# Performance work log

Measured on AMD Instinct MI355X. Metric: run time of the kernel, lower is better.

## Reference

```python
import jax, jax.numpy as jnp
import numpy as np


def setup_inputs() -> dict:
    key = jax.random.key(0)
    k1, k2, k3 = jax.random.split(key, 3)
    B, T, D = 2, 2048, 1024
    x = jax.random.normal(k1, (B, T, D), dtype=jnp.float32)
    w_qkv = jax.random.normal(k2, (3 * D, D), dtype=jnp.float32) * (D ** -0.5)
    w_out = jax.random.normal(k3, (D, D), dtype=jnp.float32) * (D ** -0.5)
    return {"x": x, "w_qkv": w_qkv, "w_out": w_out, "heads": 16}


def reference(x, w_qkv, w_out, heads):
    # SelfAttention forward: attention_type='sdp', position_mode='alibi', causal=True, eval mode.
    B, T, D = x.shape
    H = heads
    hd = D // H
    scale = hd ** -0.5

    # qkv projection: torch Linear -> x @ W^T
    qkv = (x @ w_qkv.T).reshape(B, T, 3, H, hd)
    qkv = jnp.transpose(qkv, (2, 0, 3, 1, 4))  # [3, B, H, T, hd]
    q, k, v = qkv[0], qkv[1], qkv[2]

    # ALiBi relative bias: slopes = 1 / 2^(h/H) for h = 1..H
    slopes = 1.0 / jnp.power(2.0, jnp.arange(1, H + 1, dtype=jnp.float32) / H)
    pos = jnp.arange(T, dtype=jnp.float32)
    rel = jnp.abs(pos[:, None] - pos[None, :])  # [T, T]
    bias = -slopes[None, :, None, None] * rel[None, None, :, :]  # [1, H, T, T]

    # scores + causal mask + softmax (manual path since position_bias is not None)
    scores = jnp.einsum('bhqd,bhkd->bhqk', q, k) * scale + bias
    causal_mask = jnp.triu(jnp.ones((T, T), dtype=bool), k=1)
    scores = jnp.where(causal_mask[None, None, :, :], -jnp.inf, scores)
    attn = jax.nn.softmax(scores, axis=-1)
    attn = jnp.where(jnp.isnan(attn), 1.0 / float(max(T, 1)), attn)

    out = jnp.einsum('bhqk,bhkd->bhqd', attn, v)  # [B, H, T, hd]
    out = jnp.transpose(out, (0, 2, 1, 3)).reshape(B, T, D)
    return out @ w_out.T
```

## Files before the change

### kernel.cpp

```cpp
#include <hip/hip_runtime.h>
#include <hip/hip_bf16.h>

typedef __attribute__((ext_vector_type(8))) short shortx8;
typedef __attribute__((ext_vector_type(4))) float floatx4;
typedef __attribute__((ext_vector_type(4))) unsigned uintx4;
typedef __attribute__((ext_vector_type(2))) unsigned uintx2;

#define B_ 2
#define T_ 2048
#define D_ 1024
#define H_ 16
#define HD_ 64
#define SCALE 0.125f
#define QSCALE 0.18033688011112042f
#define SMAX2 23.083120654223414f
#define FULLH ((size_t)B_ * H_ * T_ * HD_)

#define GLDS16(g, l) __builtin_amdgcn_global_load_lds( \
    (__attribute__((address_space(1))) void*)(g), \
    (__attribute__((address_space(3))) void*)(l), 16, 0, 0)

__device__ __forceinline__ short f2bf(float f) {
    union { float f; unsigned u; } v; v.f = f;
    unsigned r = v.u + 0x7FFFu + ((v.u >> 16) & 1u);
    return (short)(r >> 16);
}

__device__ __forceinline__ unsigned pk2(float x, float y) {
    union { __hip_bfloat162 h; unsigned u; } t;
    t.h = __float22bfloat162_rn(make_float2(x, y));
    return t.u;
}

__device__ __forceinline__ shortx8 cvt8(floatx4 a, floatx4 b) {
    uintx4 r = { pk2(a[0], a[1]), pk2(a[2], a[3]), pk2(b[0], b[1]), pk2(b[2], b[3]) };
    return __builtin_bit_cast(shortx8, r);
}

__device__ __forceinline__ float ex2(float x) {
#if __has_builtin(__builtin_amdgcn_exp2f)
    return __builtin_amdgcn_exp2f(x);
#else
    return exp2f(x);
#endif
}

__global__ __launch_bounds__(256) void cvt_xw(const float* __restrict__ x,
                                              const float* __restrict__ wqkv,
                                              short* __restrict__ xbf,
                                              short* __restrict__ wbf) {
    int i = blockIdx.x * 256 + threadIdx.x;
    const float* src; short* dst; int o;
    if (i < 524288) { src = x; dst = xbf; o = i; }
    else            { src = wqkv; dst = wbf; o = i - 524288; }
    const floatx4* p = reinterpret_cast<const floatx4*>(src) + (size_t)o * 2;
    *(reinterpret_cast<shortx8*>(dst) + o) = cvt8(p[0], p[1]);
}


__global__ __launch_bounds__(256) void qkv_fast(const short* __restrict__ xbf,
                                                const short* __restrict__ wbf,
                                                short* __restrict__ qout,
                                                short* __restrict__ kv) {
    __shared__ __align__(16) short As[128 * 64];
    __shared__ __align__(16) short Bs[128 * 64];

    const int tid = threadIdx.x;
    const int wv = tid >> 6;
    const int l  = tid & 63;
    const int ln = l & 15;
    const int quad = l >> 4;
    const int rowb = quad << 2;
    const int wm = wv >> 1, wn = wv & 1;
    const int m0 = blockIdx.y * 128;
    const int n0g = blockIdx.x * 128;

    const int lr = l >> 3, lc = l & 7;
    const int gcol = (lc ^ lr) << 3;
    const short* agp = xbf + (size_t)(m0 + wv * 32 + lr) * D_ + gcol;
    const short* bgp = wbf + (size_t)(n0g + wv * 32 + lr) * D_ + gcol;
    short* aldsb = As + wv * 32 * 64;
    short* bldsb = Bs + wv * 32 * 64;

    floatx4 acc[4][4] = {};

    for (int k0 = 0; k0 < D_; k0 += 64) {
        __syncthreads();
#pragma unroll
        for (int c = 0; c < 4; ++c) {
            GLDS16(agp + (size_t)(c * 8) * D_ + k0, aldsb + c * 512);
            GLDS16(bgp + (size_t)(c * 8) * D_ + k0, bldsb + c * 512);
        }
        __syncthreads();

#pragma unroll
        for (int kk = 0; kk < 2; ++kk) {
            const int csw = (kk << 2) + quad;
            const int sw = (csw ^ (ln & 7)) << 3;
            shortx8 af[4], bf[4];
#pragma unroll
            for (int i = 0; i < 4; ++i)
                af[i] = *reinterpret_cast<const shortx8*>(&As[((wm * 64 + i * 16 + ln) << 6) + sw]);
#pragma unroll
            for (int j = 0; j < 4; ++j)
                bf[j] = *reinterpret_cast<const shortx8*>(&Bs[((wn * 64 + j * 16 + ln) << 6) + sw]);
#pragma unroll
            for (int i = 0; i < 4; ++i)
#pragma unroll
                for (int j = 0; j < 4; ++j)
                    acc[i][j] = __builtin_amdgcn_mfma_f32_16x16x32_bf16(af[i], bf[j], acc[i][j], 0, 0, 0);
        }
    }

    const int sel = n0g >> 10;
    const int bb = m0 >> 11;
    const int t0w = (m0 + wm * 64) & (T_ - 1);
    const int h = ((n0g + wn * 64) >> 6) & 15;

    if (sel < 2) {
        short* dst = (sel == 0) ? qout : kv;
        const float sc = (sel == 0) ? QSCALE : 1.0f;
        const size_t hb = (size_t)(bb * H_ + h) * T_;
#pragma unroll
        for (int i = 0; i < 4; ++i)
#pragma unroll
            for (int r = 0; r < 4; ++r) {
                int t = t0w + i * 16 + rowb + r;
#pragma unroll
                for (int j = 0; j < 4; ++j)
                    dst[(hb + t) * HD_ + j * 16 + ln] = f2bf(acc[i][j][r] * sc);
            }
    } else {
        __syncthreads();
        short* tb = (wv < 2) ? (As + wv * 4096) : (Bs + (wv - 2) * 4096);
        short* vhead = kv + FULLH + (size_t)(bb * H_ + h) * HD_ * T_;
        const int dl = l & 31, th = (l >> 5) << 5;
#pragma unroll
        for (int p = 0; p < 2; ++p) {
#pragma unroll
            for (int i = 0; i < 4; ++i)
#pragma unroll
                for (int jj = 0; jj < 2; ++jj) {
                    int j = 2 * p + jj;
#pragma unroll
                    for (int r = 0; r < 4; ++r)
                        tb[(jj * 16 + ln) * 72 + i * 16 + rowb + r] = f2bf(acc[i][j][r]);
                }
            short* vd = vhead + (size_t)(p * 32 + dl) * T_ + t0w + th;
#pragma unroll
            for (int seg = 0; seg < 4; ++seg)
                *reinterpret_cast<shortx8*>(vd + seg * 8) =
                    *reinterpret_cast<const shortx8*>(&tb[dl * 72 + th + seg * 8]);
        }
    }
}

__global__ __launch_bounds__(256) void out_fast(const short* __restrict__ Abf,
                                                const short* __restrict__ wbf,
                                                float* __restrict__ out) {
    __shared__ __align__(16) short As[128 * 64];
    __shared__ __align__(16) short Bs[128 * 64];

    const int tid = threadIdx.x;
    const int wv = tid >> 6;
    const int l  = tid & 63;
    const int ln = l & 15;
    const int quad = l >> 4;
    const int rowb = quad << 2;
    const int wm = wv >> 1, wn = wv & 1;
    const int m0 = blockIdx.y * 128;
    const int n0g = blockIdx.x * 128;

    const int lr = l >> 3, lc = l & 7;
    const int gcol = (lc ^ lr) << 3;
    const short* bgp = wbf + (size_t)(n0g + wv * 32 + lr) * D_ + gcol;
    short* aldsb = As + wv * 32 * 64;
    short* bldsb = Bs + wv * 32 * 64;

    size_t abase[4];
#pragma unroll
    for (int c = 0; c < 4; ++c) {
        int m = m0 + wv * 32 + c * 8 + lr;
        int bb2 = m >> 11, t = m & (T_ - 1);
        abase[c] = ((size_t)(bb2 * H_) * T_ + t) * HD_ + gcol;
    }

    floatx4 acc[4][4] = {};

    for (int k0 = 0; k0 < D_; k0 += 64) {
        const size_t hoff = (size_t)(k0 >> 6) * T_ * HD_;
        __syncthreads();
#pragma unroll
        for (int c = 0; c < 4; ++c) {
            GLDS16(Abf + abase[c] + hoff, aldsb + c * 512);
            GLDS16(bgp + (size_t)(c * 8) * D_ + k0, bldsb + c * 512);
        }
        __syncthreads();

#pragma unroll
        for (int kk = 0; kk < 2; ++kk) {
            const int csw = (kk << 2) + quad;
            const int sw = (csw ^ (ln & 7)) << 3;
            shortx8 af[4], bf[4];
#pragma unroll
            for (int i = 0; i < 4; ++i)
                af[i] = *reinterpret_cast<const shortx8*>(&As[((wm * 64 + i * 16 + ln) << 6) + sw]);
#pragma unroll
            for (int j = 0; j < 4; ++j)
                bf[j] = *reinterpret_cast<const shortx8*>(&Bs[((wn * 64 + j * 16 + ln) << 6) + sw]);
#pragma unroll
            for (int i = 0; i < 4; ++i)
#pragma unroll
                for (int j = 0; j < 4; ++j)
                    acc[i][j] = __builtin_amdgcn_mfma_f32_16x16x32_bf16(af[i], bf[j], acc[i][j], 0, 0, 0);
        }
    }

#pragma unroll
    for (int i = 0; i < 4; ++i)
#pragma unroll
        for (int r = 0; r < 4; ++r) {
            int m = m0 + wm * 64 + i * 16 + rowb + r;
#pragma unroll
            for (int j = 0; j < 4; ++j)
                out[(size_t)m * D_ + n0g + wn * 64 + j * 16 + ln] = acc[i][j][r];
        }
}

__global__ __launch_bounds__(256, 4) void attn(const short* __restrict__ qws,
                                               const short* __restrict__ kv,
                                               short* ao,
                                               const float* __restrict__ wout,
                                               short* __restrict__ wobf) {
    if (blockIdx.x >= 1024) {
        int i = (blockIdx.x - 1024) * 256 + threadIdx.x;
        const floatx4* p = reinterpret_cast<const floatx4*>(wout) + (size_t)i * 2;
        *(reinterpret_cast<shortx8*>(wobf) + i) = cvt8(p[0], p[1]);
        return;
    }

    __shared__ __align__(16) short Ks[64][72];
    __shared__ __align__(16) short Vt[64][72];
    __shared__ __align__(16) short Pt[4][64][18];

    const int tid = threadIdx.x;
    const int wv   = tid >> 6;
    const int l    = tid & 63;
    const int ln   = l & 15;
    const int quad = l >> 4;
    const int qd   = quad << 3;
    const int rowb = quad << 2;

    const int xcd  = blockIdx.x & 7;
    const int slot = blockIdx.x >> 3;
    const int bh   = xcd * 4 + (slot & 3);
    const int qb   = 31 - (slot >> 2);
    const int h    = bh & 15;
    const int b    = bh >> 4;

    const float slope2 = 1.4426950408889634f * exp2f(-(float)(h + 1) * 0.0625f);
    const size_t koff = (size_t)(b * H_ + h) * T_ * HD_;
    const int q0 = qb * 64 + wv * 16;

    shortx8 qf[2];
#pragma unroll
    for (int kk = 0; kk < 2; ++kk)
        qf[kk] = *reinterpret_cast<const shortx8*>(&qws[koff + (size_t)(q0 + ln) * HD_ + kk * 32 + qd]);

    const int r0 = tid >> 3, c0 = (tid & 7) << 3, r1 = r0 + 32;
    const short* kbase = kv + koff;
    const short* vbase = kv + FULLH + koff;
    shortx8 kA, kB, vA, vB;
    auto FETCH = [&](int kb) {
        const short* kp = kbase + ((size_t)(kb * 64) << 6);
        kA = *reinterpret_cast<const shortx8*>(kp + ((size_t)r0 << 6) + c0);
        kB = *reinterpret_cast<const shortx8*>(kp + ((size_t)r1 << 6) + c0);
        const short* vp = vbase + kb * 64;
        vA = *reinterpret_cast<const shortx8*>(vp + ((size_t)r0 << 11) + c0);
        vB = *reinterpret_cast<const shortx8*>(vp + ((size_t)r1 << 11) + c0);
    };

    floatx4 oacc[4] = {};
    floatx4 lsum = {};
    const shortx8 ones = {16256, 16256, 16256, 16256, 16256, 16256, 16256, 16256};
    const float base0 = -SMAX2 - slope2 * (float)(q0 + rowb);

    float sncr[4][4];
#pragma unroll
    for (int nc = 0; nc < 4; ++nc)
#pragma unroll
        for (int r = 0; r < 4; ++r)
            sncr[nc][r] = slope2 * (float)(nc * 16 - r);

    FETCH(0);
    for (int kb = 0; kb <= qb; ++kb) {
        __syncthreads();
        *reinterpret_cast<shortx8*>(&Ks[r0][c0]) = kA;
        *reinterpret_cast<shortx8*>(&Ks[r1][c0]) = kB;
        *reinterpret_cast<shortx8*>(&Vt[r0][c0]) = vA;
        *reinterpret_cast<shortx8*>(&Vt[r1][c0]) = vB;
        __syncthreads();
        if (kb < qb) FETCH(kb + 1);

        const bool diag = (kb == qb);
        const int kln = kb * 64 + ln;
        const float bb0 = slope2 * (float)kln + base0;

        if (!diag) {
#pragma unroll
            for (int nc = 0; nc < 4; ++nc) {
                floatx4 s = {};
#pragma unroll
                for (int kk = 0; kk < 2; ++kk) {
                    shortx8 bfr = *reinterpret_cast<const shortx8*>(&Ks[nc * 16 + ln][kk * 32 + qd]);
                    s = __builtin_amdgcn_mfma_f32_16x16x32_bf16(qf[kk], bfr, s, 0, 0, 0);
                }
                unsigned w0 = pk2(ex2(s[0] + (bb0 + sncr[nc][0])),
                                  ex2(s[1] + (bb0 + sncr[nc][1])));
                unsigned w1 = pk2(ex2(s[2] + (bb0 + sncr[nc][2])),
                                  ex2(s[3] + (bb0 + sncr[nc][3])));
                short* pp = &Pt[wv][nc * 16 + ln][rowb];
                *reinterpret_cast<unsigned*>(pp) = w0;
                *reinterpret_cast<unsigned*>(pp + 2) = w1;
            }
        } else {
            const int ncmax = wv + 1;
#pragma unroll
            for (int nc = 0; nc < 4; ++nc) {
                floatx4 s = {};
                if (nc < ncmax) {
#pragma unroll
                    for (int kk = 0; kk < 2; ++kk) {
                        shortx8 bfr = *reinterpret_cast<const shortx8*>(&Ks[nc * 16 + ln][kk * 32 + qd]);
                        s = __builtin_amdgcn_mfma_f32_16x16x32_bf16(qf[kk], bfr, s, 0, 0, 0);
                    }
                }
                float p[4];
#pragma unroll
                for (int r = 0; r < 4; ++r) {
                    bool ok = (kln + nc * 16) <= (q0 + rowb + r);
                    float e = ex2(s[r] + (bb0 + sncr[nc][r]));
                    p[r] = ok ? e : 0.0f;
                }
                unsigned w0 = pk2(p[0], p[1]);
                unsigned w1 = pk2(p[2], p[3]);
                short* pp = &Pt[wv][nc * 16 + ln][rowb];
                *reinterpret_cast<unsigned*>(pp) = w0;
                *reinterpret_cast<unsigned*>(pp + 2) = w1;
            }
        }

        __builtin_amdgcn_s_setprio(1);
#pragma unroll
        for (int kk = 0; kk < 2; ++kk) {
            if (diag && kk * 32 > wv * 16 + 15) continue;
            shortx8 pf;
#pragma unroll
            for (int j = 0; j < 8; ++j) pf[j] = Pt[wv][kk * 32 + qd + j][ln];
            lsum = __builtin_amdgcn_mfma_f32_16x16x32_bf16(pf, ones, lsum, 0, 0, 0);
#pragma unroll
            for (int nc = 0; nc < 4; ++nc) {
                shortx8 bfr = *reinterpret_cast<const shortx8*>(&Vt[nc * 16 + ln][kk * 32 + qd]);
                oacc[nc] = __builtin_amdgcn_mfma_f32_16x16x32_bf16(pf, bfr, oacc[nc], 0, 0, 0);
            }
        }
        __builtin_amdgcn_s_setprio(0);
    }

#pragma unroll
    for (int r = 0; r < 4; ++r) {
        float inv = 1.0f / lsum[r];
        int t = q0 + rowb + r;
#pragma unroll
        for (int nc = 0; nc < 4; ++nc)
            ao[koff + (size_t)t * HD_ + nc * 16 + ln] = f2bf(oacc[nc][r] * inv);
    }
}

__global__ __launch_bounds__(256) void qkv_slow(const float* __restrict__ x,
                                                const float* __restrict__ wqkv,
                                                short* __restrict__ qout,
                                                short* __restrict__ kv) {
    __shared__ __align__(16) short As[64][72];
    __shared__ __align__(16) short Bs[64][72];
    const int tid = threadIdx.x;
    const int wv = tid >> 6, l = tid & 63, ln = l & 15, quad = l >> 4, qd = quad << 3;
    const int m0 = blockIdx.y * 64;
    const int sel = blockIdx.x >> 4, h = blockIdx.x & 15;
    const int nrow = sel * D_ + h * HD_;
    const int sr0 = tid >> 3, sc0 = (tid & 7) << 3, sr1 = sr0 + 32;
    floatx4 fa[4], fb[4];
    auto FETCH = [&](int k0) {
        const float* ap = &x[(size_t)(m0 + sr0) * D_ + k0 + sc0];
        fa[0] = *reinterpret_cast<const floatx4*>(ap);
        fa[1] = *reinterpret_cast<const floatx4*>(ap + 4);
        ap += (size_t)32 * D_;
        fa[2] = *reinterpret_cast<const floatx4*>(ap);
        fa[3] = *reinterpret_cast<const floatx4*>(ap + 4);
        const float* bp = &wqkv[(size_t)(nrow + sr0) * D_ + k0 + sc0];
        fb[0] = *reinterpret_cast<const floatx4*>(bp);
        fb[1] = *reinterpret_cast<const floatx4*>(bp + 4);
        bp += (size_t)32 * D_;
        fb[2] = *reinterpret_cast<const floatx4*>(bp);
        fb[3] = *reinterpret_cast<const floatx4*>(bp + 4);
    };
    floatx4 acc[4] = {};
    FETCH(0);
    for (int k0 = 0; k0 < D_; k0 += 64) {
        __syncthreads();
        *reinterpret_cast<shortx8*>(&As[sr0][sc0]) = cvt8(fa[0], fa[1]);
        *reinterpret_cast<shortx8*>(&As[sr1][sc0]) = cvt8(fa[2], fa[3]);
        *reinterpret_cast<shortx8*>(&Bs[sr0][sc0]) = cvt8(fb[0], fb[1]);
        *reinterpret_cast<shortx8*>(&Bs[sr1][sc0]) = cvt8(fb[2], fb[3]);
        __syncthreads();
        if (k0 + 64 < D_) FETCH(k0 + 64);
        const int mr = (wv << 4) + ln;
#pragma unroll
        for (int kk = 0; kk < 2; ++kk) {
            shortx8 a = *reinterpret_cast<const shortx8*>(&As[mr][kk * 32 + qd]);
#pragma unroll
            for (int nc = 0; nc < 4; ++nc) {
                shortx8 b = *reinterpret_cast<const shortx8*>(&Bs[nc * 16 + ln][kk * 32 + qd]);
                acc[nc] = __builtin_amdgcn_mfma_f32_16x16x32_bf16(a, b, acc[nc], 0, 0, 0);
            }
        }
    }
    const int bb = m0 >> 11, t0 = m0 & (T_ - 1);
    if (sel < 2) {
        short* dst = (sel == 0) ? qout : kv;
        const float sc = (sel == 0) ? QSCALE : 1.0f;
#pragma unroll
        for (int r = 0; r < 4; ++r) {
            int t = t0 + (wv << 4) + (quad << 2) + r;
#pragma unroll
            for (int nc = 0; nc < 4; ++nc)
                dst[((size_t)(bb * H_ + h) * T_ + t) * HD_ + nc * 16 + ln] = f2bf(acc[nc][r] * sc);
        }
    } else {
        __syncthreads();
#pragma unroll
        for (int r = 0; r < 4; ++r)
#pragma unroll
            for (int nc = 0; nc < 4; ++nc)
                As[nc * 16 + ln][(wv << 4) + (quad << 2) + r] = f2bf(acc[nc][r]);
        __syncthreads();
        const int d = tid >> 2, tseg = (tid & 3) << 4;
        short* vdst = kv + FULLH + ((size_t)(bb * H_ + h) * HD_ + d) * T_ + t0 + tseg;
        *reinterpret_cast<shortx8*>(vdst)     = *reinterpret_cast<const shortx8*>(&As[d][tseg]);
        *reinterpret_cast<shortx8*>(vdst + 8) = *reinterpret_cast<const shortx8*>(&As[d][tseg + 8]);
    }
}

__global__ __launch_bounds__(256) void out_slow(const short* __restrict__ A,
                                                const float* __restrict__ W,
                                                float* __restrict__ out) {
    __shared__ __align__(16) short As[64][72];
    __shared__ __align__(16) short Bs[64][72];
    const int tid = threadIdx.x;
    const int wv = tid >> 6, l = tid & 63, ln = l & 15, quad = l >> 4, qd = quad << 3;
    const int m0 = blockIdx.y * 64, n0 = blockIdx.x * 64;
    const int sr0 = tid >> 3, sc0 = (tid & 7) << 3, sr1 = sr0 + 32;
    shortx8 sa0, sa1;
    floatx4 fb[4];
    auto FETCH = [&](int k0) {
        const int h = k0 >> 6;
        int m = m0 + sr0;
        int bb = m >> 11, t = m & (T_ - 1);
        sa0 = *reinterpret_cast<const shortx8*>(A + ((size_t)(bb * H_ + h) * T_ + t) * HD_ + sc0);
        m = m0 + sr1; bb = m >> 11; t = m & (T_ - 1);
        sa1 = *reinterpret_cast<const shortx8*>(A + ((size_t)(bb * H_ + h) * T_ + t) * HD_ + sc0);
        const float* bp = &W[(size_t)(n0 + sr0) * D_ + k0 + sc0];
        fb[0] = *reinterpret_cast<const floatx4*>(bp);
        fb[1] = *reinterpret_cast<const floatx4*>(bp + 4);
        bp += (size_t)32 * D_;
        fb[2] = *reinterpret_cast<const floatx4*>(bp);
        fb[3] = *reinterpret_cast<const floatx4*>(bp + 4);
    };
    floatx4 acc[4] = {};
    FETCH(0);
    for (int k0 = 0; k0 < D_; k0 += 64) {
        __syncthreads();
        *reinterpret_cast<shortx8*>(&As[sr0][sc0]) = sa0;
        *reinterpret_cast<shortx8*>(&As[sr1][sc0]) = sa1;
        *reinterpret_cast<shortx8*>(&Bs[sr0][sc0]) = cvt8(fb[0], fb[1]);
        *reinterpret_cast<shortx8*>(&Bs[sr1][sc0]) = cvt8(fb[2], fb[3]);
        __syncthreads();
        if (k0 + 64 < D_) FETCH(k0 + 64);
        const int mr = (wv << 4) + ln;
#pragma unroll
        for (int kk = 0; kk < 2; ++kk) {
            shortx8 a = *reinterpret_cast<const shortx8*>(&As[mr][kk * 32 + qd]);
#pragma unroll
            for (int nc = 0; nc < 4; ++nc) {
                shortx8 b = *reinterpret_cast<const shortx8*>(&Bs[nc * 16 + ln][kk * 32 + qd]);
                acc[nc] = __builtin_amdgcn_mfma_f32_16x16x32_bf16(a, b, acc[nc], 0, 0, 0);
            }
        }
    }
#pragma unroll
    for (int r = 0; r < 4; ++r) {
        int m = m0 + (wv << 4) + (quad << 2) + r;
#pragma unroll
        for (int nc = 0; nc < 4; ++nc)
            out[(size_t)m * D_ + n0 + nc * 16 + ln] = acc[nc][r];
    }
}

extern "C" void kernel_launch(void* const* d_in, const int* in_sizes, int n_in,
                              void* d_out, int out_size, void* d_ws, size_t ws_size,
                              hipStream_t stream) {
    const float* x    = (const float*)d_in[0];
    const float* wqkv = (const float*)d_in[1];
    const float* wout = (const float*)d_in[2];

    short* kvbuf = (short*)d_out;
    float* out   = (float*)d_out;

    if (ws_size >= 23068672ULL) {
        short* xbf  = (short*)d_ws;
        short* wbf  = xbf + 4 * 1024 * 1024;
        short* qws  = xbf + 7 * 1024 * 1024;
        short* wobf = xbf;

        cvt_xw<<<3584, 256, 0, stream>>>(x, wqkv, xbf, wbf);
        qkv_fast<<<dim3(24, 32), 256, 0, stream>>>(xbf, wbf, qws, kvbuf);
        attn<<<dim3(1536), 256, 0, stream>>>(qws, kvbuf, qws, wout, wobf);
        out_fast<<<dim3(8, 32), 256, 0, stream>>>(qws, wobf, out);
    } else {
        short* qws = (short*)d_ws;
        qkv_slow<<<dim3(48, 64), 256, 0, stream>>>(x, wqkv, qws, kvbuf);
        attn<<<dim3(1024), 256, 0, stream>>>(qws, kvbuf, qws, nullptr, nullptr);
        out_slow<<<dim3(16, 64), 256, 0, stream>>>(qws, wout, out);
    }
}
```

Baseline: 184.9 us.

## Pair high and low causal query blocks per attention workgroup

Each attention workgroup now handles two query blocks, qb and 31-qb, from the same head, so every workgroup does the same amount of causal work. Each staged K/V tile is reused for both query blocks, which halves the K/V LDS staging and global loads per query. The cost is more live registers (two sets of accumulators and Q fragments) and half as many workgroups, which could hurt occupancy and latency hiding. Grid sizes and the weight-conversion block offset are updated to match.

```diff
diff --git a/kernel.cpp b/kernel.cpp
--- a/kernel.cpp
+++ b/kernel.cpp
@@ -232,8 +232,8 @@
                                                short* ao,
                                                const float* __restrict__ wout,
                                                short* __restrict__ wobf) {
-    if (blockIdx.x >= 1024) {
-        int i = (blockIdx.x - 1024) * 256 + threadIdx.x;
+    if (blockIdx.x >= 512) {
+        int i = (blockIdx.x - 512) * 256 + threadIdx.x;
         const floatx4* p = reinterpret_cast<const floatx4*>(wout) + (size_t)i * 2;
         *(reinterpret_cast<shortx8*>(wobf) + i) = cvt8(p[0], p[1]);
         return;
@@ -241,7 +241,8 @@
 
     __shared__ __align__(16) short Ks[64][72];
     __shared__ __align__(16) short Vt[64][72];
-    __shared__ __align__(16) short Pt[4][64][18];
+    __shared__ __align__(16) short PtH[4][64][20];
+    __shared__ __align__(16) short PtL[4][64][20];
 
     const int tid = threadIdx.x;
     const int wv   = tid >> 6;
@@ -254,18 +255,23 @@
     const int xcd  = blockIdx.x & 7;
     const int slot = blockIdx.x >> 3;
     const int bh   = xcd * 4 + (slot & 3);
-    const int qb   = 31 - (slot >> 2);
+    const int pr   = slot >> 2;
+    const int qbH  = 31 - pr;
+    const int qbL  = pr;
     const int h    = bh & 15;
     const int b    = bh >> 4;
 
     const float slope2 = 1.4426950408889634f * exp2f(-(float)(h + 1) * 0.0625f);
     const size_t koff = (size_t)(b * H_ + h) * T_ * HD_;
-    const int q0 = qb * 64 + wv * 16;
-
-    shortx8 qf[2];
-#pragma unroll
-    for (int kk = 0; kk < 2; ++kk)
-        qf[kk] = *reinterpret_cast<const shortx8*>(&qws[koff + (size_t)(q0 + ln) * HD_ + kk * 32 + qd]);
+    const int q0H = qbH * 64 + wv * 16;
+    const int q0L = qbL * 64 + wv * 16;
+
+    shortx8 qfH[2], qfL[2];
+#pragma unroll
+    for (int kk = 0; kk < 2; ++kk) {
+        qfH[kk] = *reinterpret_cast<const shortx8*>(&qws[koff + (size_t)(q0H + ln) * HD_ + kk * 32 + qd]);
+        qfL[kk] = *reinterpret_cast<const shortx8*>(&qws[koff + (size_t)(q0L + ln) * HD_ + kk * 32 + qd]);
+    }
 
     const int r0 = tid >> 3, c0 = (tid & 7) << 3, r1 = r0 + 32;
     const short* kbase = kv + koff;
@@ -280,88 +286,104 @@
         vB = *reinterpret_cast<const shortx8*>(vp + ((size_t)r1 << 11) + c0);
     };
 
-    floatx4 oacc[4] = {};
-    floatx4 lsum = {};
+    floatx4 oaccH[4] = {}, oaccL[4] = {};
+    floatx4 lsumH = {}, lsumL = {};
     const shortx8 ones = {16256, 16256, 16256, 16256, 16256, 16256, 16256, 16256};
-    const float base0 = -SMAX2 - slope2 * (float)(q0 + rowb);
-
-    float sncr[4][4];
-#pragma unroll
-    for (int nc = 0; nc < 4; ++nc)
-#pragma unroll
-        for (int r = 0; r < 4; ++r)
-            sncr[nc][r] = slope2 * (float)(nc * 16 - r);
+    const float base0H = -SMAX2 - slope2 * (float)(q0H + rowb);
+    const float base0L = -SMAX2 - slope2 * (float)(q0L + rowb);
+    float snc16[4];
+#pragma unroll
+    for (int nc = 0; nc < 4; ++nc) snc16[nc] = slope2 * (float)(nc * 16);
 
     FETCH(0);
-    for (int kb = 0; kb <= qb; ++kb) {
+    for (int kb = 0; kb <= qbH; ++kb) {
         __syncthreads();
         *reinterpret_cast<shortx8*>(&Ks[r0][c0]) = kA;
         *reinterpret_cast<shortx8*>(&Ks[r1][c0]) = kB;
         *reinterpret_cast<shortx8*>(&Vt[r0][c0]) = vA;
         *reinterpret_cast<shortx8*>(&Vt[r1][c0]) = vB;
         __syncthreads();
-        if (kb < qb) FETCH(kb + 1);
-
-        const bool diag = (kb == qb);
+        if (kb < qbH) FETCH(kb + 1);
+
+        const bool diagH = (kb == qbH);
+        const bool liveL = (kb <= qbL);
+        const bool diagL = (kb == qbL);
         const int kln = kb * 64 + ln;
-        const float bb0 = slope2 * (float)kln + base0;
-
-        if (!diag) {
-#pragma unroll
-            for (int nc = 0; nc < 4; ++nc) {
-                floatx4 s = {};
-#pragma unroll
-                for (int kk = 0; kk < 2; ++kk) {
-                    shortx8 bfr = *reinterpret_cast<const shortx8*>(&Ks[nc * 16 + ln][kk * 32 + qd]);
-                    s = __builtin_amdgcn_mfma_f32_16x16x32_bf16(qf[kk], bfr, s, 0, 0, 0);
-                }
-                unsigned w0 = pk2(ex2(s[0] + (bb0 + sncr[nc][0])),
-                                  ex2(s[1] + (bb0 + sncr[nc][1])));
-                unsigned w1 = pk2(ex2(s[2] + (bb0 + sncr[nc][2])),
-                                  ex2(s[3] + (bb0 + sncr[nc][3])));
-                short* pp = &Pt[wv][nc * 16 + ln][rowb];
-                *reinterpret_cast<unsigned*>(pp) = w0;
-                *reinterpret_cast<unsigned*>(pp + 2) = w1;
-            }
-        } else {
-            const int ncmax = wv + 1;
-#pragma unroll
-            for (int nc = 0; nc < 4; ++nc) {
-                floatx4 s = {};
-                if (nc < ncmax) {
-#pragma unroll
-                    for (int kk = 0; kk < 2; ++kk) {
-                        shortx8 bfr = *reinterpret_cast<const shortx8*>(&Ks[nc * 16 + ln][kk * 32 + qd]);
-                        s = __builtin_amdgcn_mfma_f32_16x16x32_bf16(qf[kk], bfr, s, 0, 0, 0);
-                    }
-                }
+        const float bb0H = slope2 * (float)kln + base0H;
+        const float bb0L = slope2 * (float)kln + base0L;
+        float bbrH[4], bbrL[4];
+#pragma unroll
+        for (int r = 0; r < 4; ++r) {
+            bbrH[r] = bb0H - slope2 * (float)r;
+            bbrL[r] = bb0L - slope2 * (float)r;
+        }
+
+#pragma unroll
+        for (int nc = 0; nc < 4; ++nc) {
+            floatx4 sH = {}, sL = {};
+            const bool doH = !diagH || (nc <= wv);
+            const bool doL = liveL && (!diagL || (nc <= wv));
+#pragma unroll
+            for (int kk = 0; kk < 2; ++kk) {
+                shortx8 bfr = *reinterpret_cast<const shortx8*>(&Ks[nc * 16 + ln][kk * 32 + qd]);
+                if (doH) sH = __builtin_amdgcn_mfma_f32_16x16x32_bf16(qfH[kk], bfr, sH, 0, 0, 0);
+                if (doL) sL = __builtin_amdgcn_mfma_f32_16x16x32_bf16(qfL[kk], bfr, sL, 0, 0, 0);
+            }
+            if (!diagH) {
+                uintx2 pkd = { pk2(ex2(sH[0] + bbrH[0] + snc16[nc]), ex2(sH[1] + bbrH[1] + snc16[nc])),
+                               pk2(ex2(sH[2] + bbrH[2] + snc16[nc]), ex2(sH[3] + bbrH[3] + snc16[nc])) };
+                *reinterpret_cast<uintx2*>(&PtH[wv][nc * 16 + ln][rowb]) = pkd;
+            } else {
                 float p[4];
 #pragma unroll
                 for (int r = 0; r < 4; ++r) {
-                    bool ok = (kln + nc * 16) <= (q0 + rowb + r);
-                    float e = ex2(s[r] + (bb0 + sncr[nc][r]));
+                    bool ok = (kln + nc * 16) <= (q0H + rowb + r);
+                    float e = ex2(sH[r] + bbrH[r] + snc16[nc]);
                     p[r] = ok ? e : 0.0f;
                 }
-                unsigned w0 = pk2(p[0], p[1]);
-                unsigned w1 = pk2(p[2], p[3]);
-                short* pp = &Pt[wv][nc * 16 + ln][rowb];
-                *reinterpret_cast<unsigned*>(pp) = w0;
-                *reinterpret_cast<unsigned*>(pp + 2) = w1;
+                uintx2 pkd = { pk2(p[0], p[1]), pk2(p[2], p[3]) };
+                *reinterpret_cast<uintx2*>(&PtH[wv][nc * 16 + ln][rowb]) = pkd;
+            }
+            if (liveL) {
+                if (!diagL) {
+                    uintx2 pkd = { pk2(ex2(sL[0] + bbrL[0] + snc16[nc]), ex2(sL[1] + bbrL[1] + snc16[nc])),
+                                   pk2(ex2(sL[2] + bbrL[2] + snc16[nc]), ex2(sL[3] + bbrL[3] + snc16[nc])) };
+                    *reinterpret_cast<uintx2*>(&PtL[wv][nc * 16 + ln][rowb]) = pkd;
+                } else {
+                    float p[4];
+#pragma unroll
+                    for (int r = 0; r < 4; ++r) {
+                        bool ok = (kln + nc * 16) <= (q0L + rowb + r);
+                        float e = ex2(sL[r] + bbrL[r] + snc16[nc]);
+                        p[r] = ok ? e : 0.0f;
+                    }
+                    uintx2 pkd = { pk2(p[0], p[1]), pk2(p[2], p[3]) };
+                    *reinterpret_cast<uintx2*>(&PtL[wv][nc * 16 + ln][rowb]) = pkd;
+                }
             }
         }
 
         __builtin_amdgcn_s_setprio(1);
 #pragma unroll
         for (int kk = 0; kk < 2; ++kk) {
-            if (diag && kk * 32 > wv * 16 + 15) continue;
-            shortx8 pf;
-#pragma unroll
-            for (int j = 0; j < 8; ++j) pf[j] = Pt[wv][kk * 32 + qd + j][ln];
-            lsum = __builtin_amdgcn_mfma_f32_16x16x32_bf16(pf, ones, lsum, 0, 0, 0);
+            const bool skipH = diagH && (kk * 32 > wv * 16 + 15);
+            const bool goL = liveL && !(diagL && (kk * 32 > wv * 16 + 15));
+            shortx8 pfH, pfL;
+            if (!skipH) {
+#pragma unroll
+                for (int j = 0; j < 8; ++j) pfH[j] = PtH[wv][kk * 32 + qd + j][ln];
+                lsumH = __builtin_amdgcn_mfma_f32_16x16x32_bf16(pfH, ones, lsumH, 0, 0, 0);
+            }
+            if (goL) {
+#pragma unroll
+                for (int j = 0; j < 8; ++j) pfL[j] = PtL[wv][kk * 32 + qd + j][ln];
+                lsumL = __builtin_amdgcn_mfma_f32_16x16x32_bf16(pfL, ones, lsumL, 0, 0, 0);
+            }
 #pragma unroll
             for (int nc = 0; nc < 4; ++nc) {
                 shortx8 bfr = *reinterpret_cast<const shortx8*>(&Vt[nc * 16 + ln][kk * 32 + qd]);
-                oacc[nc] = __builtin_amdgcn_mfma_f32_16x16x32_bf16(pf, bfr, oacc[nc], 0, 0, 0);
+                if (!skipH) oaccH[nc] = __builtin_amdgcn_mfma_f32_16x16x32_bf16(pfH, bfr, oaccH[nc], 0, 0, 0);
+                if (goL)   oaccL[nc] = __builtin_amdgcn_mfma_f32_16x16x32_bf16(pfL, bfr, oaccL[nc], 0, 0, 0);
             }
         }
         __builtin_amdgcn_s_setprio(0);
@@ -369,11 +391,15 @@
 
 #pragma unroll
     for (int r = 0; r < 4; ++r) {
-        float inv = 1.0f / lsum[r];
-        int t = q0 + rowb + r;
-#pragma unroll
-        for (int nc = 0; nc < 4; ++nc)
-            ao[koff + (size_t)t * HD_ + nc * 16 + ln] = f2bf(oacc[nc][r] * inv);
+        float invH = 1.0f / lsumH[r];
+        float invL = 1.0f / lsumL[r];
+        int tH = q0H + rowb + r;
+        int tL = q0L + rowb + r;
+#pragma unroll
+        for (int nc = 0; nc < 4; ++nc) {
+            ao[koff + (size_t)tH * HD_ + nc * 16 + ln] = f2bf(oaccH[nc][r] * invH);
+            ao[koff + (size_t)tL * HD_ + nc * 16 + ln] = f2bf(oaccL[nc][r] * invL);
+        }
     }
 }
 
@@ -524,12 +550,12 @@
 
         cvt_xw<<<3584, 256, 0, stream>>>(x, wqkv, xbf, wbf);
         qkv_fast<<<dim3(24, 32), 256, 0, stream>>>(xbf, wbf, qws, kvbuf);
-        attn<<<dim3(1536), 256, 0, stream>>>(qws, kvbuf, qws, wout, wobf);
+        attn<<<dim3(1024), 256, 0, stream>>>(qws, kvbuf, qws, wout, wobf);
         out_fast<<<dim3(8, 32), 256, 0, stream>>>(qws, wobf, out);
     } else {
         short* qws = (short*)d_ws;
         qkv_slow<<<dim3(48, 64), 256, 0, stream>>>(x, wqkv, qws, kvbuf);
-        attn<<<dim3(1024), 256, 0, stream>>>(qws, kvbuf, qws, nullptr, nullptr);
+        attn<<<dim3(512), 256, 0, stream>>>(qws, kvbuf, qws, nullptr, nullptr);
         out_slow<<<dim3(16, 64), 256, 0, stream>>>(qws, wout, out);
     }
 }
```

New measurement: 208.5 us. 1.13x slower.

## Rewrite attention with 32x32x16 MFMA, register-resident P via permlane swap

Applied to the files above, without the earlier changes.

The attention kernel moves from four 16-row waves using 16x16x32 MFMA to two waves of 32 query rows each using 32x32x16 MFMA, with S computed transposed (K as A operand). The P tile stays in registers: v_permlane32_swap rearranges the packed bf16 probabilities into the A-operand layout, so the LDS Pt round trip and its scalar gathers are gone. Blocks shrink to 128 threads with a new query-block ordering that interleaves long and short causal rows for load balance, and the wout conversion tail uses 1024 extra 128-thread blocks. The cost is fewer waves per block, more accumulator registers, and reliance on gfx950-specific permlane instructions.

```diff
diff --git a/kernel.cpp b/kernel.cpp
--- a/kernel.cpp
+++ b/kernel.cpp
@@ -3,6 +3,7 @@
 
 typedef __attribute__((ext_vector_type(8))) short shortx8;
 typedef __attribute__((ext_vector_type(4))) float floatx4;
+typedef __attribute__((ext_vector_type(16))) float floatx16;
 typedef __attribute__((ext_vector_type(4))) unsigned uintx4;
 typedef __attribute__((ext_vector_type(2))) unsigned uintx2;
 
@@ -57,7 +58,6 @@
     *(reinterpret_cast<shortx8*>(dst) + o) = cvt8(p[0], p[1]);
 }
 
-
 __global__ __launch_bounds__(256) void qkv_fast(const short* __restrict__ xbf,
                                                 const short* __restrict__ wbf,
                                                 short* __restrict__ qout,
@@ -227,13 +227,13 @@
         }
 }
 
-__global__ __launch_bounds__(256, 4) void attn(const short* __restrict__ qws,
+__global__ __launch_bounds__(128, 2) void attn(const short* __restrict__ qws,
                                                const short* __restrict__ kv,
                                                short* ao,
                                                const float* __restrict__ wout,
                                                short* __restrict__ wobf) {
     if (blockIdx.x >= 1024) {
-        int i = (blockIdx.x - 1024) * 256 + threadIdx.x;
+        int i = (blockIdx.x - 1024) * 128 + threadIdx.x;
         const floatx4* p = reinterpret_cast<const floatx4*>(wout) + (size_t)i * 2;
         *(reinterpret_cast<shortx8*>(wobf) + i) = cvt8(p[0], p[1]);
         return;
@@ -241,139 +241,130 @@
 
     __shared__ __align__(16) short Ks[64][72];
     __shared__ __align__(16) short Vt[64][72];
-    __shared__ __align__(16) short Pt[4][64][18];
 
     const int tid = threadIdx.x;
-    const int wv   = tid >> 6;
-    const int l    = tid & 63;
-    const int ln   = l & 15;
-    const int quad = l >> 4;
-    const int qd   = quad << 3;
-    const int rowb = quad << 2;
-
-    const int xcd  = blockIdx.x & 7;
-    const int slot = blockIdx.x >> 3;
-    const int bh   = xcd * 4 + (slot & 3);
-    const int qb   = 31 - (slot >> 2);
-    const int h    = bh & 15;
-    const int b    = bh >> 4;
+    const int wv = tid >> 6;
+    const int l  = tid & 63;
+    const int ql = l & 31;
+    const int hi = l >> 5;
+
+    const int id  = blockIdx.x;
+    const int xcd = id & 7;
+    const int u2  = (id >> 3) & 3;
+    const int rr  = (id >> 5) & 7;
+    const int tt  = id >> 8;
+    const int bh  = xcd * 4 + u2;
+    const int qblk = (tt == 0) ? 31 - rr : (tt == 1) ? rr : (tt == 2) ? 23 - rr : 8 + rr;
+    const int h = bh & 15, b = bh >> 4;
 
     const float slope2 = 1.4426950408889634f * exp2f(-(float)(h + 1) * 0.0625f);
     const size_t koff = (size_t)(b * H_ + h) * T_ * HD_;
-    const int q0 = qb * 64 + wv * 16;
-
-    shortx8 qf[2];
-#pragma unroll
-    for (int kk = 0; kk < 2; ++kk)
-        qf[kk] = *reinterpret_cast<const shortx8*>(&qws[koff + (size_t)(q0 + ln) * HD_ + kk * 32 + qd]);
-
-    const int r0 = tid >> 3, c0 = (tid & 7) << 3, r1 = r0 + 32;
+    const int q0w = qblk * 64 + wv * 32;
+
+    shortx8 qf[4];
+#pragma unroll
+    for (int ds = 0; ds < 4; ++ds)
+        qf[ds] = *reinterpret_cast<const shortx8*>(&qws[koff + (size_t)(q0w + ql) * HD_ + ds * 16 + hi * 8]);
+
+    const float cbase = slope2 * (float)(4 * hi - (q0w + ql)) - SMAX2;
+    float rb[16];
+#pragma unroll
+    for (int g = 0; g < 16; ++g)
+        rb[g] = cbase + slope2 * (float)((g & 3) + 8 * (g >> 2));
+    const float s32 = slope2 * 32.0f;
+
+    const int sr = tid >> 1;
+    const int sc = (tid & 1) << 5;
     const short* kbase = kv + koff;
     const short* vbase = kv + FULLH + koff;
-    shortx8 kA, kB, vA, vB;
+    shortx8 kR[4], vR[4];
     auto FETCH = [&](int kb) {
-        const short* kp = kbase + ((size_t)(kb * 64) << 6);
-        kA = *reinterpret_cast<const shortx8*>(kp + ((size_t)r0 << 6) + c0);
-        kB = *reinterpret_cast<const shortx8*>(kp + ((size_t)r1 << 6) + c0);
-        const short* vp = vbase + kb * 64;
-        vA = *reinterpret_cast<const shortx8*>(vp + ((size_t)r0 << 11) + c0);
-        vB = *reinterpret_cast<const shortx8*>(vp + ((size_t)r1 << 11) + c0);
+        const short* kp = kbase + (((size_t)(kb * 64 + sr)) << 6) + sc;
+        const short* vp = vbase + (size_t)sr * T_ + kb * 64 + sc;
+#pragma unroll
+        for (int s = 0; s < 4; ++s) {
+            kR[s] = *reinterpret_cast<const shortx8*>(kp + 8 * s);
+            vR[s] = *reinterpret_cast<const shortx8*>(vp + 8 * s);
+        }
     };
 
-    floatx4 oacc[4] = {};
-    floatx4 lsum = {};
+    floatx16 oacc0 = {}, oacc1 = {}, lsum = {};
     const shortx8 ones = {16256, 16256, 16256, 16256, 16256, 16256, 16256, 16256};
-    const float base0 = -SMAX2 - slope2 * (float)(q0 + rowb);
-
-    float sncr[4][4];
-#pragma unroll
-    for (int nc = 0; nc < 4; ++nc)
-#pragma unroll
-        for (int r = 0; r < 4; ++r)
-            sncr[nc][r] = slope2 * (float)(nc * 16 - r);
+    const int qlh = ql - 4 * hi;
 
     FETCH(0);
-    for (int kb = 0; kb <= qb; ++kb) {
-        __syncthreads();
-        *reinterpret_cast<shortx8*>(&Ks[r0][c0]) = kA;
-        *reinterpret_cast<shortx8*>(&Ks[r1][c0]) = kB;
-        *reinterpret_cast<shortx8*>(&Vt[r0][c0]) = vA;
-        *reinterpret_cast<shortx8*>(&Vt[r1][c0]) = vB;
-        __syncthreads();
-        if (kb < qb) FETCH(kb + 1);
-
-        const bool diag = (kb == qb);
-        const int kln = kb * 64 + ln;
-        const float bb0 = slope2 * (float)kln + base0;
-
-        if (!diag) {
-#pragma unroll
-            for (int nc = 0; nc < 4; ++nc) {
-                floatx4 s = {};
-#pragma unroll
-                for (int kk = 0; kk < 2; ++kk) {
-                    shortx8 bfr = *reinterpret_cast<const shortx8*>(&Ks[nc * 16 + ln][kk * 32 + qd]);
-                    s = __builtin_amdgcn_mfma_f32_16x16x32_bf16(qf[kk], bfr, s, 0, 0, 0);
+    for (int kb = 0; kb <= qblk; ++kb) {
+        __syncthreads();
+#pragma unroll
+        for (int s = 0; s < 4; ++s) {
+            *reinterpret_cast<shortx8*>(&Ks[sr][sc + 8 * s]) = kR[s];
+            *reinterpret_cast<shortx8*>(&Vt[sr][sc + 8 * s]) = vR[s];
+        }
+        __syncthreads();
+        if (kb < qblk) FETCH(kb + 1);
+
+        const bool diag = (kb == qblk);
+        const float tb = slope2 * (float)(kb * 64);
+
+#pragma unroll
+        for (int nc = 0; nc < 2; ++nc) {
+            const bool act = !diag || (nc == 0) || (wv == 1);
+            if (!act) continue;
+            const bool part = diag && (nc == wv);
+
+            floatx16 s = {};
+#pragma unroll
+            for (int ds = 0; ds < 4; ++ds) {
+                shortx8 kf = *reinterpret_cast<const shortx8*>(&Ks[nc * 32 + ql][ds * 16 + hi * 8]);
+                s = __builtin_amdgcn_mfma_f32_32x32x16_bf16(kf, qf[ds], s, 0, 0, 0);
+            }
+
+            const float tnc = tb + (nc ? s32 : 0.0f);
+            float p[16];
+#pragma unroll
+            for (int g = 0; g < 16; ++g) {
+                float e = ex2(s[g] + rb[g] + tnc);
+                if (part) {
+                    const int kc = (g & 3) + 8 * (g >> 2);
+                    e = (kc <= qlh) ? e : 0.0f;
                 }
-                unsigned w0 = pk2(ex2(s[0] + (bb0 + sncr[nc][0])),
-                                  ex2(s[1] + (bb0 + sncr[nc][1])));
-                unsigned w1 = pk2(ex2(s[2] + (bb0 + sncr[nc][2])),
-                                  ex2(s[3] + (bb0 + sncr[nc][3])));
-                short* pp = &Pt[wv][nc * 16 + ln][rowb];
-                *reinterpret_cast<unsigned*>(pp) = w0;
-                *reinterpret_cast<unsigned*>(pp + 2) = w1;
-            }
-        } else {
-            const int ncmax = wv + 1;
-#pragma unroll
-            for (int nc = 0; nc < 4; ++nc) {
-                floatx4 s = {};
-                if (nc < ncmax) {
-#pragma unroll
-                    for (int kk = 0; kk < 2; ++kk) {
-                        shortx8 bfr = *reinterpret_cast<const shortx8*>(&Ks[nc * 16 + ln][kk * 32 + qd]);
-                        s = __builtin_amdgcn_mfma_f32_16x16x32_bf16(qf[kk], bfr, s, 0, 0, 0);
-                    }
-                }
-                float p[4];
-#pragma unroll
-                for (int r = 0; r < 4; ++r) {
-                    bool ok = (kln + nc * 16) <= (q0 + rowb + r);
-                    float e = ex2(s[r] + (bb0 + sncr[nc][r]));
-                    p[r] = ok ? e : 0.0f;
-                }
-                unsigned w0 = pk2(p[0], p[1]);
-                unsigned w1 = pk2(p[2], p[3]);
-                short* pp = &Pt[wv][nc * 16 + ln][rowb];
-                *reinterpret_cast<unsigned*>(pp) = w0;
-                *reinterpret_cast<unsigned*>(pp + 2) = w1;
-            }
-        }
-
-        __builtin_amdgcn_s_setprio(1);
-#pragma unroll
-        for (int kk = 0; kk < 2; ++kk) {
-            if (diag && kk * 32 > wv * 16 + 15) continue;
-            shortx8 pf;
-#pragma unroll
-            for (int j = 0; j < 8; ++j) pf[j] = Pt[wv][kk * 32 + qd + j][ln];
-            lsum = __builtin_amdgcn_mfma_f32_16x16x32_bf16(pf, ones, lsum, 0, 0, 0);
-#pragma unroll
-            for (int nc = 0; nc < 4; ++nc) {
-                shortx8 bfr = *reinterpret_cast<const shortx8*>(&Vt[nc * 16 + ln][kk * 32 + qd]);
-                oacc[nc] = __builtin_amdgcn_mfma_f32_16x16x32_bf16(pf, bfr, oacc[nc], 0, 0, 0);
-            }
-        }
-        __builtin_amdgcn_s_setprio(0);
-    }
-
-#pragma unroll
-    for (int r = 0; r < 4; ++r) {
-        float inv = 1.0f / lsum[r];
-        int t = q0 + rowb + r;
-#pragma unroll
-        for (int nc = 0; nc < 4; ++nc)
-            ao[koff + (size_t)t * HD_ + nc * 16 + ln] = f2bf(oacc[nc][r] * inv);
+                p[g] = e;
+            }
+
+            unsigned cv[4][2];
+#pragma unroll
+            for (int g = 0; g < 4; ++g) {
+                cv[g][0] = pk2(p[4 * g + 0], p[4 * g + 1]);
+                cv[g][1] = pk2(p[4 * g + 2], p[4 * g + 3]);
+            }
+
+            __builtin_amdgcn_s_setprio(1);
+#pragma unroll
+            for (int kh = 0; kh < 2; ++kh) {
+                unsigned w0 = cv[2 * kh][0], w2 = cv[2 * kh + 1][0];
+                unsigned w1 = cv[2 * kh][1], w3 = cv[2 * kh + 1][1];
+                asm volatile("v_permlane32_swap_b32 %0, %1" : "+v"(w0), "+v"(w2));
+                asm volatile("v_permlane32_swap_b32 %0, %1" : "+v"(w1), "+v"(w3));
+                uintx4 uu = {w0, w1, w2, w3};
+                shortx8 apv = __builtin_bit_cast(shortx8, uu);
+                const int ks = nc * 2 + kh;
+                lsum = __builtin_amdgcn_mfma_f32_32x32x16_bf16(apv, ones, lsum, 0, 0, 0);
+                shortx8 vf0 = *reinterpret_cast<const shortx8*>(&Vt[ql][ks * 16 + hi * 8]);
+                oacc0 = __builtin_amdgcn_mfma_f32_32x32x16_bf16(apv, vf0, oacc0, 0, 0, 0);
+                shortx8 vf1 = *reinterpret_cast<const shortx8*>(&Vt[32 + ql][ks * 16 + hi * 8]);
+                oacc1 = __builtin_amdgcn_mfma_f32_32x32x16_bf16(apv, vf1, oacc1, 0, 0, 0);
+            }
+            __builtin_amdgcn_s_setprio(0);
+        }
+    }
+
+#pragma unroll
+    for (int g = 0; g < 16; ++g) {
+        const int qrow = (g & 3) + 8 * (g >> 2) + 4 * hi;
+        const float inv = 1.0f / lsum[g];
+        const size_t ob = koff + (size_t)(q0w + qrow) * HD_ + ql;
+        ao[ob]      = f2bf(oacc0[g] * inv);
+        ao[ob + 32] = f2bf(oacc1[g] * inv);
     }
 }
 
@@ -420,8 +411,8 @@
             shortx8 a = *reinterpret_cast<const shortx8*>(&As[mr][kk * 32 + qd]);
 #pragma unroll
             for (int nc = 0; nc < 4; ++nc) {
-                shortx8 b = *reinterpret_cast<const shortx8*>(&Bs[nc * 16 + ln][kk * 32 + qd]);
-                acc[nc] = __builtin_amdgcn_mfma_f32_16x16x32_bf16(a, b, acc[nc], 0, 0, 0);
+                shortx8 bq = *reinterpret_cast<const shortx8*>(&Bs[nc * 16 + ln][kk * 32 + qd]);
+                acc[nc] = __builtin_amdgcn_mfma_f32_16x16x32_bf16(a, bq, acc[nc], 0, 0, 0);
             }
         }
     }
@@ -492,8 +483,8 @@
             shortx8 a = *reinterpret_cast<const shortx8*>(&As[mr][kk * 32 + qd]);
 #pragma unroll
             for (int nc = 0; nc < 4; ++nc) {
-                shortx8 b = *reinterpret_cast<const shortx8*>(&Bs[nc * 16 + ln][kk * 32 + qd]);
-                acc[nc] = __builtin_amdgcn_mfma_f32_16x16x32_bf16(a, b, acc[nc], 0, 0, 0);
+                shortx8 bq = *reinterpret_cast<const shortx8*>(&Bs[nc * 16 + ln][kk * 32 + qd]);
+                acc[nc] = __builtin_amdgcn_mfma_f32_16x16x32_bf16(a, bq, acc[nc], 0, 0, 0);
             }
         }
     }
@@ -524,12 +515,12 @@
 
         cvt_xw<<<3584, 256, 0, stream>>>(x, wqkv, xbf, wbf);
         qkv_fast<<<dim3(24, 32), 256, 0, stream>>>(xbf, wbf, qws, kvbuf);
-        attn<<<dim3(1536), 256, 0, stream>>>(qws, kvbuf, qws, wout, wobf);
+        attn<<<dim3(2048), 128, 0, stream>>>(qws, kvbuf, qws, wout, wobf);
         out_fast<<<dim3(8, 32), 256, 0, stream>>>(qws, wobf, out);
     } else {
         short* qws = (short*)d_ws;
         qkv_slow<<<dim3(48, 64), 256, 0, stream>>>(x, wqkv, qws, kvbuf);
-        attn<<<dim3(1024), 256, 0, stream>>>(qws, kvbuf, qws, nullptr, nullptr);
+        attn<<<dim3(1024), 128, 0, stream>>>(qws, kvbuf, qws, nullptr, nullptr);
         out_slow<<<dim3(16, 64), 256, 0, stream>>>(qws, wout, out);
     }
 }
```

Result: no change. 182.0 us (-1.5%).
